# Kernel tuning notes

Measured on AMD Instinct MI355X. Metric: run time of the kernel, lower is better.

## Reference

```python
import jax, jax.numpy as jnp
import numpy as np

N = 100000
E = 1600000
IN_F = 128
OUT_F = 128
EPS = 1e-12


def setup_inputs() -> dict:
    key = jax.random.key(0)
    k1, k2, k3, k4, k5, k6 = jax.random.split(key, 6)
    x = jax.random.normal(k1, (N, IN_F), dtype=jnp.float32)
    rows = jnp.sort(jax.random.randint(k2, (E,), 0, N, dtype=jnp.int32))
    cols = jax.random.randint(k3, (E,), 0, N, dtype=jnp.int32)
    vals = jax.random.uniform(k4, (E,), dtype=jnp.float32)
    # nn.Linear(2*in_features, out_features): W is [out, 2*in], b is [out]
    bound = 1.0 / np.sqrt(2 * IN_F)
    W = jax.random.uniform(k5, (OUT_F, 2 * IN_F), dtype=jnp.float32, minval=-bound, maxval=bound)
    b = jax.random.uniform(k6, (OUT_F,), dtype=jnp.float32, minval=-bound, maxval=bound)
    return {"x": x, "rows": rows, "cols": cols, "vals": vals, "W": W, "b": b}


def reference(x, rows, cols, vals, W, b):
    # spmm(adj, x): gather source-node features, scale by edge weight,
    # segment-sum into destination rows.
    gathered = vals[:, None] * x[cols]                      # [E, in]
    neighbor = jax.ops.segment_sum(gathered, rows, num_segments=N)  # [N, in]
    combined = jnp.concatenate([x, neighbor], axis=1)       # [N, 2*in]
    out = combined @ W.T + b                                # [N, out]
    # F.normalize(out, p=2, dim=1): divide by max(||row||_2, eps)
    norm = jnp.sqrt(jnp.sum(out * out, axis=1, keepdims=True))
    return out / jnp.maximum(norm, EPS)
```

## Files before the change

### kernel.cpp

```cpp
#include <hip/hip_runtime.h>
#include <hip/hip_bf16.h>


typedef __bf16 bf16x8_t __attribute__((ext_vector_type(8)));
typedef float f32x4_t __attribute__((ext_vector_type(4)));
typedef float f32x2_t __attribute__((ext_vector_type(2)));
typedef unsigned int u32x2_t __attribute__((ext_vector_type(2)));

#define DESC_CAP 512
#define RING_D   8

__device__ __forceinline__ unsigned int f32_to_bf16(float f) {
    unsigned int u = __float_as_uint(f);
    unsigned int r = u + 0x7fffu + ((u >> 16) & 1u);
    return r >> 16;
}
__device__ __forceinline__ unsigned int pack2(float a, float b) {
    return f32_to_bf16(a) | (f32_to_bf16(b) << 16);
}

__global__ void prep_kernel(const float* __restrict__ x, u32x2_t* __restrict__ xq,
                            float* __restrict__ xs,
                            const int* __restrict__ rows, int* __restrict__ row_ptr,
                            const float* __restrict__ W, uint4* __restrict__ Wf,
                            int Nn, int Ee, int xcast_blks, int rowptr_blks) {
    int blk = blockIdx.x;
    if (blk < xcast_blks) {
        int lane = threadIdx.x & 63;
        int wv   = threadIdx.x >> 6;
        int r    = blk * 16 + wv * 4 + (lane >> 4);
        int fc   = (lane & 15) * 8;
        if (r < Nn) {
            const f32x4_t* pf = (const f32x4_t*)(x + (size_t)r * 128 + fc);
            f32x4_t f0 = __builtin_nontemporal_load(pf);
            f32x4_t f1 = __builtin_nontemporal_load(pf + 1);
            float m = fmaxf(fmaxf(fmaxf(fabsf(f0.x), fabsf(f0.y)),
                                  fmaxf(fabsf(f0.z), fabsf(f0.w))),
                            fmaxf(fmaxf(fabsf(f1.x), fabsf(f1.y)),
                                  fmaxf(fabsf(f1.z), fabsf(f1.w))));
            m = fmaxf(m, __shfl_xor(m, 1, 64));
            m = fmaxf(m, __shfl_xor(m, 2, 64));
            m = fmaxf(m, __shfl_xor(m, 4, 64));
            m = fmaxf(m, __shfl_xor(m, 8, 64));
            float inv = (m > 0.f) ? 127.f / m : 0.f;
            int q0 = (int)rintf(f0.x * inv), q1 = (int)rintf(f0.y * inv);
            int q2 = (int)rintf(f0.z * inv), q3 = (int)rintf(f0.w * inv);
            int q4 = (int)rintf(f1.x * inv), q5 = (int)rintf(f1.y * inv);
            int q6 = (int)rintf(f1.z * inv), q7 = (int)rintf(f1.w * inv);
            u32x2_t o;
            o.x = (q0 & 255) | ((q1 & 255) << 8) | ((q2 & 255) << 16)
                | ((unsigned)(q3 & 255) << 24);
            o.y = (q4 & 255) | ((q5 & 255) << 8) | ((q6 & 255) << 16)
                | ((unsigned)(q7 & 255) << 24);
            __builtin_nontemporal_store(o, &xq[(size_t)r * 16 + (lane & 15)]);
            if ((lane & 15) == 0) xs[r] = m * (1.f / 127.f);
        }
    } else if (blk < xcast_blks + rowptr_blks) {
        int n = (blk - xcast_blks) * 256 + threadIdx.x;
        if (n <= Nn) {
            int lo = 0, hi = Ee;
            while (lo < hi) {
                int mid = (lo + hi) >> 1;
                if (rows[mid] < n) lo = mid + 1; else hi = mid;
            }
            row_ptr[n] = lo;
        }
    } else {
        int i = (blk - xcast_blks - rowptr_blks) * 256 + threadIdx.x;
        int lane = i & 63, ks = (i >> 6) & 7, t = i >> 9;
        int row = t * 16 + (lane & 15);
        int col = ks * 32 + (lane >> 4) * 8;
        const float* p = W + (size_t)row * 256 + col;
        uint4 o;
        o.x = pack2(p[0], p[1]); o.y = pack2(p[2], p[3]);
        o.z = pack2(p[4], p[5]); o.w = pack2(p[6], p[7]);
        Wf[i] = o;
    }
}

__global__ void __launch_bounds__(256, 6)
fused_kernel(const int* __restrict__ row_ptr,
             const int* __restrict__ cols,
             const float* __restrict__ vals,
             const float* __restrict__ x,
             const float* __restrict__ xs,
             const char* __restrict__ xqB,
             const bf16x8_t* __restrict__ Wf,
             const float* __restrict__ b,
             float* __restrict__ out, int Nn) {
    __shared__ int   rpS[17];
    __shared__ uint2 cvLDS[DESC_CAP];
    __shared__ uint4 nbLDS[16 * 17];
    __shared__ float __attribute__((aligned(16))) sqLDS[16][4];

    int lane = threadIdx.x & 63;
    int w    = threadIdx.x >> 6;
    int r0   = blockIdx.x * 16;

    if (threadIdx.x < 17)
        rpS[threadIdx.x] = row_ptr[min(r0 + (int)threadIdx.x, Nn)];
    __syncthreads();

    int eLo = rpS[0], eHi = rpS[16];
    int cnt = eHi - eLo;
    bool big = cnt > DESC_CAP;

    if (!big) {
        for (int i = threadIdx.x; i < cnt; i += 256) {
            int e = eLo + i;
            int c = __builtin_nontemporal_load(&cols[e]);
            float v = __builtin_nontemporal_load(&vals[e]);
            float vw = v * xs[c];
            int d = (e >= rpS[8]) ? 8 : 0;
            d += (e >= rpS[d + 4]) ? 4 : 0;
            d += (e >= rpS[d + 2]) ? 2 : 0;
            d += (e >= rpS[d + 1]) ? 1 : 0;
            uint2 cv;
            cv.x = (unsigned)c | ((unsigned)d << 28);
            cv.y = __float_as_uint(vw);
            cvLDS[i] = cv;
        }
    }
    {
        unsigned* nz = (unsigned*)nbLDS;
        for (int i = threadIdx.x; i < 16 * 17 * 4; i += 256) nz[i] = 0u;
    }
    __syncthreads();

    if (!big) {
        int wLo = __builtin_amdgcn_readfirstlane(rpS[w * 4]     - eLo);
        int wHi = __builtin_amdgcn_readfirstlane(rpS[w * 4 + 4] - eLo);
        int nEd = wHi - wLo;
        if (nEd > 0) {
            unsigned lane2 = (unsigned)lane << 1;
            int wHiM1 = wHi - 1;
            unsigned* nbW = (unsigned*)nbLDS;

            unsigned P[RING_D];
            uint2    cv[RING_D];
#pragma unroll
            for (int d = 0; d < RING_D; ++d) {
                int kd = min(wLo + d, wHiM1);
                cv[d] = cvLDS[kd];
                unsigned voff = ((cv[d].x & 0x0FFFFFFFu) << 7) | lane2;
                P[d] = *(const unsigned short*)(xqB + voff);
            }
            int cur = (int)(cv[0].x >> 28);
            float ax = 0.f, ay = 0.f;

            int nit = (nEd + RING_D - 1) / RING_D;
            int k0 = wLo;
            for (int it = 0; it < nit; ++it, k0 += RING_D) {
#pragma unroll
                for (int d = 0; d < RING_D; ++d) {
                    int k = k0 + d;
                    uint2 cvk = cv[d];
                    int dk = (int)(cvk.x >> 28);
                    if (dk != cur) {
                        nbW[cur * 68 + lane] = pack2(ax, ay);
                        ax = 0.f; ay = 0.f;
                        cur = dk;
                    }
                    float vv = (k < wHi) ? __uint_as_float(cvk.y) : 0.f;
                    unsigned Pd = P[d];
                    float fx = (float)(int)(signed char)(Pd & 0xffu);
                    float fy = (float)(int)(signed char)((Pd >> 8) & 0xffu);
                    ax += vv * fx;
                    ay += vv * fy;
                    uint2 cvn = cvLDS[min(k + RING_D, wHiM1)];
                    unsigned voff = ((cvn.x & 0x0FFFFFFFu) << 7) | lane2;
                    P[d] = *(const unsigned short*)(xqB + voff);
                    cv[d] = cvn;
                }
            }
            nbW[cur * 68 + lane] = pack2(ax, ay);
        }
    } else {
        int h = lane >> 4;
        int l = lane & 15;
        int node = w * 4 + h;
        int n = r0 + node;
        int nn = min(n, Nn - 1);
        int start = row_ptr[nn], end = row_ptr[nn + 1];
        if (n >= Nn) end = start;
        unsigned loff = (unsigned)l << 3;

        f32x2_t a0 = {0.f, 0.f}, a1 = {0.f, 0.f}, a2 = {0.f, 0.f}, a3 = {0.f, 0.f};
        for (int e = start; e < end; ++e) {
            int   c = cols[e];
            float v = vals[e] * xs[c];
            uint2 p = *(const uint2*)(xqB + (((unsigned)c << 7) | loff));
            a0.x += v * (float)(int)(signed char)(p.x & 0xffu);
            a0.y += v * (float)(int)(signed char)((p.x >> 8) & 0xffu);
            a1.x += v * (float)(int)(signed char)((p.x >> 16) & 0xffu);
            a1.y += v * (float)(int)(signed char)(p.x >> 24);
            a2.x += v * (float)(int)(signed char)(p.y & 0xffu);
            a2.y += v * (float)(int)(signed char)((p.y >> 8) & 0xffu);
            a3.x += v * (float)(int)(signed char)((p.y >> 16) & 0xffu);
            a3.y += v * (float)(int)(signed char)(p.y >> 24);
        }
        uint4 o;
        o.x = pack2(a0.x, a0.y); o.y = pack2(a1.x, a1.y);
        o.z = pack2(a2.x, a2.y); o.w = pack2(a3.x, a3.y);
        nbLDS[node * 17 + l] = o;
    }
    __syncthreads();

    int m    = lane & 15;
    int quad = lane >> 4;

    int arow = min(r0 + m, Nn - 1);
    const float* xrow = x + (size_t)arow * 128;

    bf16x8_t a[8];
#pragma unroll
    for (int ks = 0; ks < 4; ++ks) {
        const f32x4_t* pf = (const f32x4_t*)(xrow + 32 * ks + 8 * quad);
        f32x4_t f0 = pf[0];
        f32x4_t f1 = pf[1];
        union { bf16x8_t v; unsigned u[4]; } au;
        au.u[0] = pack2(f0.x, f0.y); au.u[1] = pack2(f0.z, f0.w);
        au.u[2] = pack2(f1.x, f1.y); au.u[3] = pack2(f1.z, f1.w);
        a[ks] = au.v;
    }
#pragma unroll
    for (int ks = 0; ks < 4; ++ks)
        a[4 + ks] = *(const bf16x8_t*)&nbLDS[m * 17 + ks * 4 + quad];

    f32x4_t acc[2];
    float bc[2];
#pragma unroll
    for (int j = 0; j < 2; ++j) {
        int t = w * 2 + j;
        acc[j] = (f32x4_t){0.f, 0.f, 0.f, 0.f};
        bc[j]  = b[t * 16 + m];
#pragma unroll
        for (int ks = 0; ks < 8; ++ks) {
            acc[j] = __builtin_amdgcn_mfma_f32_16x16x32_bf16(
                a[ks], Wf[(t * 8 + ks) * 64 + lane], acc[j], 0, 0, 0);
        }
    }

    float sq[4] = {0.f, 0.f, 0.f, 0.f};
#pragma unroll
    for (int j = 0; j < 2; ++j)
#pragma unroll
        for (int r = 0; r < 4; ++r) {
            float u = acc[j][r] + bc[j];
            sq[r] += u * u;
        }
#pragma unroll
    for (int off = 1; off <= 8; off <<= 1) {
#pragma unroll
        for (int r = 0; r < 4; ++r) sq[r] += __shfl_xor(sq[r], off, 64);
    }
    if (m == 0) {
#pragma unroll
        for (int r = 0; r < 4; ++r) sqLDS[quad * 4 + r][w] = sq[r];
    }
    __syncthreads();

    float scale[4];
#pragma unroll
    for (int r = 0; r < 4; ++r) {
        const float4 q4 = *(const float4*)sqLDS[quad * 4 + r];
        float tot = q4.x + q4.y + q4.z + q4.w;
        scale[r] = 1.f / fmaxf(sqrtf(tot), 1e-12f);
    }

#pragma unroll
    for (int r = 0; r < 4; ++r) {
        int row = r0 + quad * 4 + r;
        if (row < Nn) {
            float* orow = out + (size_t)row * 128;
#pragma unroll
            for (int j = 0; j < 2; ++j) {
                int t = w * 2 + j;
                __builtin_nontemporal_store((acc[j][r] + bc[j]) * scale[r],
                                            &orow[t * 16 + m]);
            }
        }
    }
}

extern "C" void kernel_launch(void* const* d_in, const int* in_sizes, int n_in,
                              void* d_out, int out_size, void* d_ws, size_t ws_size,
                              hipStream_t stream) {
    const float* x    = (const float*)d_in[0];
    const int*   rows = (const int*)  d_in[1];
    const int*   cols = (const int*)  d_in[2];
    const float* vals = (const float*)d_in[3];
    const float* W    = (const float*)d_in[4];
    const float* b    = (const float*)d_in[5];
    float*       out  = (float*)d_out;

    const int Nn = in_sizes[0] / 128;
    const int Ee = in_sizes[1];

    char*    ws      = (char*)d_ws;
    int*     row_ptr = (int*)ws;
    uint4*   Wf      = (uint4*)(ws + 448 * 1024);
    float*   xs      = (float*)(ws + 512 * 1024);
    u32x2_t* xq      = (u32x2_t*)(ws + 1024 * 1024);

    const int xcast_blks  = (Nn + 15) / 16;
    const int rowptr_blks = (Nn + 1 + 255) / 256;
    const int wcast_blks  = 16;

    prep_kernel<<<xcast_blks + rowptr_blks + wcast_blks, 256, 0, stream>>>(
        x, xq, xs, rows, row_ptr, W, Wf, Nn, Ee, xcast_blks, rowptr_blks);
    fused_kernel<<<(Nn + 15) / 16, 256, 0, stream>>>(
        row_ptr, cols, vals, x, xs, (const char*)xq,
        (const bf16x8_t*)Wf, b, out, Nn);
}
```

Baseline: 202.1 us.

## Precompute bf16 copy of x and per-edge scaled weights in separate passes

The prep kernel now also writes a bf16 copy of x, so the fused kernel reads 256 bytes per row for its self-feature MFMA operand instead of converting fp32. A new vw_kernel precomputes vals*xs[col] per edge, which takes the random xs gather out of the fused kernel's edge staging. This adds an extra kernel launch, an extra full pass over cols and vals, and about 26MB of extra writes and reads for the bf16 copy.

```diff
diff --git a/kernel.cpp b/kernel.cpp
--- a/kernel.cpp
+++ b/kernel.cpp
@@ -6,6 +6,7 @@
 typedef float f32x4_t __attribute__((ext_vector_type(4)));
 typedef float f32x2_t __attribute__((ext_vector_type(2)));
 typedef unsigned int u32x2_t __attribute__((ext_vector_type(2)));
+typedef unsigned int u32x4_t __attribute__((ext_vector_type(4)));
 
 #define DESC_CAP 512
 #define RING_D   8
@@ -18,8 +19,12 @@
 __device__ __forceinline__ unsigned int pack2(float a, float b) {
     return f32_to_bf16(a) | (f32_to_bf16(b) << 16);
 }
-
-__global__ void prep_kernel(const float* __restrict__ x, u32x2_t* __restrict__ xq,
+__device__ __forceinline__ float bflo(unsigned int p) { return __uint_as_float(p << 16); }
+__device__ __forceinline__ float bfhi(unsigned int p) { return __uint_as_float(p & 0xffff0000u); }
+
+__global__ void prep_kernel(const float* __restrict__ x,
+                            u32x4_t* __restrict__ xb4,
+                            u32x2_t* __restrict__ xq8,
                             float* __restrict__ xs,
                             const int* __restrict__ rows, int* __restrict__ row_ptr,
                             const float* __restrict__ W, uint4* __restrict__ Wf,
@@ -29,11 +34,15 @@
         int lane = threadIdx.x & 63;
         int wv   = threadIdx.x >> 6;
         int r    = blk * 16 + wv * 4 + (lane >> 4);
-        int fc   = (lane & 15) * 8;
+        int l    = lane & 15;
         if (r < Nn) {
-            const f32x4_t* pf = (const f32x4_t*)(x + (size_t)r * 128 + fc);
+            const f32x4_t* pf = (const f32x4_t*)(x + (size_t)r * 128 + l * 8);
             f32x4_t f0 = __builtin_nontemporal_load(pf);
             f32x4_t f1 = __builtin_nontemporal_load(pf + 1);
+            u32x4_t ob;
+            ob.x = pack2(f0.x, f0.y); ob.y = pack2(f0.z, f0.w);
+            ob.z = pack2(f1.x, f1.y); ob.w = pack2(f1.z, f1.w);
+            __builtin_nontemporal_store(ob, &xb4[(size_t)r * 16 + l]);
             float m = fmaxf(fmaxf(fmaxf(fabsf(f0.x), fabsf(f0.y)),
                                   fmaxf(fabsf(f0.z), fabsf(f0.w))),
                             fmaxf(fmaxf(fabsf(f1.x), fabsf(f1.y)),
@@ -47,13 +56,13 @@
             int q2 = (int)rintf(f0.z * inv), q3 = (int)rintf(f0.w * inv);
             int q4 = (int)rintf(f1.x * inv), q5 = (int)rintf(f1.y * inv);
             int q6 = (int)rintf(f1.z * inv), q7 = (int)rintf(f1.w * inv);
-            u32x2_t o;
-            o.x = (q0 & 255) | ((q1 & 255) << 8) | ((q2 & 255) << 16)
-                | ((unsigned)(q3 & 255) << 24);
-            o.y = (q4 & 255) | ((q5 & 255) << 8) | ((q6 & 255) << 16)
-                | ((unsigned)(q7 & 255) << 24);
-            __builtin_nontemporal_store(o, &xq[(size_t)r * 16 + (lane & 15)]);
-            if ((lane & 15) == 0) xs[r] = m * (1.f / 127.f);
+            u32x2_t oq;
+            oq.x = (q0 & 255) | ((q1 & 255) << 8) | ((q2 & 255) << 16)
+                 | ((unsigned)(q3 & 255) << 24);
+            oq.y = (q4 & 255) | ((q5 & 255) << 8) | ((q6 & 255) << 16)
+                 | ((unsigned)(q7 & 255) << 24);
+            __builtin_nontemporal_store(oq, &xq8[(size_t)r * 16 + l]);
+            if (l == 0) xs[r] = m * (1.f / 127.f);
         }
     } else if (blk < xcast_blks + rowptr_blks) {
         int n = (blk - xcast_blks) * 256 + threadIdx.x;
@@ -78,12 +87,30 @@
     }
 }
 
+__global__ void vw_kernel(const int* __restrict__ cols,
+                          const float* __restrict__ vals,
+                          const float* __restrict__ xs,
+                          float* __restrict__ vw, int Ee) {
+    int i = (blockIdx.x * 256 + (int)threadIdx.x) * 4;
+    if (i + 3 < Ee) {
+        u32x4_t c4 = __builtin_nontemporal_load((const u32x4_t*)(cols + i));
+        f32x4_t v4 = __builtin_nontemporal_load((const f32x4_t*)(vals + i));
+        f32x4_t o;
+        o.x = v4.x * xs[c4.x];
+        o.y = v4.y * xs[c4.y];
+        o.z = v4.z * xs[c4.z];
+        o.w = v4.w * xs[c4.w];
+        __builtin_nontemporal_store(o, (f32x4_t*)(vw + i));
+    } else {
+        for (int e = i; e < Ee; ++e) vw[e] = vals[e] * xs[cols[e]];
+    }
+}
+
 __global__ void __launch_bounds__(256, 6)
 fused_kernel(const int* __restrict__ row_ptr,
              const int* __restrict__ cols,
-             const float* __restrict__ vals,
-             const float* __restrict__ x,
-             const float* __restrict__ xs,
+             const float* __restrict__ vw,
+             const char* __restrict__ xbB,
              const char* __restrict__ xqB,
              const bf16x8_t* __restrict__ Wf,
              const float* __restrict__ b,
@@ -109,15 +136,14 @@
         for (int i = threadIdx.x; i < cnt; i += 256) {
             int e = eLo + i;
             int c = __builtin_nontemporal_load(&cols[e]);
-            float v = __builtin_nontemporal_load(&vals[e]);
-            float vw = v * xs[c];
+            float v = __builtin_nontemporal_load(&vw[e]);
             int d = (e >= rpS[8]) ? 8 : 0;
             d += (e >= rpS[d + 4]) ? 4 : 0;
             d += (e >= rpS[d + 2]) ? 2 : 0;
             d += (e >= rpS[d + 1]) ? 1 : 0;
             uint2 cv;
             cv.x = (unsigned)c | ((unsigned)d << 28);
-            cv.y = __float_as_uint(vw);
+            cv.y = __float_as_uint(v);
             cvLDS[i] = cv;
         }
     }
@@ -188,7 +214,7 @@
         f32x2_t a0 = {0.f, 0.f}, a1 = {0.f, 0.f}, a2 = {0.f, 0.f}, a3 = {0.f, 0.f};
         for (int e = start; e < end; ++e) {
             int   c = cols[e];
-            float v = vals[e] * xs[c];
+            float v = vw[e];
             uint2 p = *(const uint2*)(xqB + (((unsigned)c << 7) | loff));
             a0.x += v * (float)(int)(signed char)(p.x & 0xffu);
             a0.y += v * (float)(int)(signed char)((p.x >> 8) & 0xffu);
@@ -210,19 +236,11 @@
     int quad = lane >> 4;
 
     int arow = min(r0 + m, Nn - 1);
-    const float* xrow = x + (size_t)arow * 128;
+    const bf16x8_t* Ax = (const bf16x8_t*)(xbB + (size_t)arow * 256);
 
     bf16x8_t a[8];
 #pragma unroll
-    for (int ks = 0; ks < 4; ++ks) {
-        const f32x4_t* pf = (const f32x4_t*)(xrow + 32 * ks + 8 * quad);
-        f32x4_t f0 = pf[0];
-        f32x4_t f1 = pf[1];
-        union { bf16x8_t v; unsigned u[4]; } au;
-        au.u[0] = pack2(f0.x, f0.y); au.u[1] = pack2(f0.z, f0.w);
-        au.u[2] = pack2(f1.x, f1.y); au.u[3] = pack2(f1.z, f1.w);
-        a[ks] = au.v;
-    }
+    for (int ks = 0; ks < 4; ++ks) a[ks] = Ax[ks * 4 + quad];
 #pragma unroll
     for (int ks = 0; ks < 4; ++ks)
         a[4 + ks] = *(const bf16x8_t*)&nbLDS[m * 17 + ks * 4 + quad];
@@ -301,15 +319,20 @@
     int*     row_ptr = (int*)ws;
     uint4*   Wf      = (uint4*)(ws + 448 * 1024);
     float*   xs      = (float*)(ws + 512 * 1024);
-    u32x2_t* xq      = (u32x2_t*)(ws + 1024 * 1024);
+    float*   vw      = (float*)(ws + 1024 * 1024);
+    u32x4_t* xb      = (u32x4_t*)(ws + 8 * 1024 * 1024);
+    u32x2_t* xq      = (u32x2_t*)(ws + 34 * 1024 * 1024);
 
     const int xcast_blks  = (Nn + 15) / 16;
     const int rowptr_blks = (Nn + 1 + 255) / 256;
     const int wcast_blks  = 16;
+    const int vw_blks     = (Ee / 4 + 255) / 256;
+    const int grid        = (Nn + 15) / 16;
 
     prep_kernel<<<xcast_blks + rowptr_blks + wcast_blks, 256, 0, stream>>>(
-        x, xq, xs, rows, row_ptr, W, Wf, Nn, Ee, xcast_blks, rowptr_blks);
-    fused_kernel<<<(Nn + 15) / 16, 256, 0, stream>>>(
-        row_ptr, cols, vals, x, xs, (const char*)xq,
+        x, xb, xq, xs, rows, row_ptr, W, Wf, Nn, Ee, xcast_blks, rowptr_blks);
+    vw_kernel<<<vw_blks, 256, 0, stream>>>(cols, vals, xs, vw, Ee);
+    fused_kernel<<<grid, 256, 0, stream>>>(
+        row_ptr, cols, vw, (const char*)xb, (const char*)xq,
         (const bf16x8_t*)Wf, b, out, Nn);
 }
```

Measured after the change: 208.8 us. 3.3% more time.
